# Optimization experiments

Measured on AMD Instinct MI355X. Metric: run time of the kernel, lower is better.

Reference implementation:

```python
import jax, jax.numpy as jnp
import numpy as np

D_MODEL = 1024
H = 16
D_K = D_MODEL // H


def setup_inputs() -> dict:
    key = jax.random.key(0)
    ks = jax.random.split(key, 12)
    B, S = 2, 2048
    inp = {
        "q": jax.random.normal(ks[0], (B, S, D_MODEL), jnp.float32),
        "k": jax.random.normal(ks[1], (B, S, D_MODEL), jnp.float32),
        "v": jax.random.normal(ks[2], (B, S, D_MODEL), jnp.float32),
        "mask": jax.random.randint(ks[3], (1, 1, S, S), 0, 2, jnp.int32),
    }
    s = 1.0 / np.sqrt(D_MODEL)
    inp["wq_w"] = jax.random.normal(ks[4], (D_MODEL, D_MODEL), jnp.float32) * s
    inp["wq_b"] = jnp.zeros((D_MODEL,), jnp.float32)
    inp["wk_w"] = jax.random.normal(ks[5], (D_MODEL, D_MODEL), jnp.float32) * s
    inp["wk_b"] = jnp.zeros((D_MODEL,), jnp.float32)
    inp["wv_w"] = jax.random.normal(ks[6], (D_MODEL, D_MODEL), jnp.float32) * s
    inp["wv_b"] = jnp.zeros((D_MODEL,), jnp.float32)
    inp["wo_w"] = jax.random.normal(ks[7], (D_MODEL, D_MODEL), jnp.float32) * s
    inp["wo_b"] = jnp.zeros((D_MODEL,), jnp.float32)
    return inp


def reference(q, k, v, mask, wq_w, wq_b, wk_w, wk_b, wv_w, wv_b, wo_w, wo_b):
    B, S, _ = q.shape
    # projections (torch Linear: x @ W^T + b)
    def proj(x, w, b):
        y = x @ w.T + b
        return y.reshape(B, S, H, D_K).transpose(0, 2, 1, 3)  # [B,H,S,Dk]

    Q = proj(q, wq_w, wq_b)
    K = proj(k, wk_w, wk_b)
    V = proj(v, wv_w, wv_b)

    scores = jnp.einsum("bhqd,bhkd->bhqk", Q, K) / jnp.sqrt(jnp.float32(D_K))
    # source quirk: masked positions set to 1e-9 (NOT -inf) before softmax
    scores = jnp.where(mask == 0, jnp.float32(1e-9), scores)
    attn = jax.nn.softmax(scores, axis=-1)
    out = jnp.einsum("bhqk,bhkd->bhqd", attn, V)
    out = out.transpose(0, 2, 1, 3).reshape(B, S, H * D_K)
    return out @ wo_w.T + wo_b
```

## Files before the change

kernel.cpp:

```cpp
#include <hip/hip_runtime.h>

typedef _Float16 half_t;
typedef _Float16 h8 __attribute__((ext_vector_type(8)));
typedef _Float16 h4 __attribute__((ext_vector_type(4)));
typedef _Float16 h2 __attribute__((ext_vector_type(2)));
typedef float f32x4 __attribute__((ext_vector_type(4)));
typedef float f32x16 __attribute__((ext_vector_type(16)));

#define S_LEN 2048
#define DMODEL 1024
#define NHEAD 16
#define HDK 64
#define NB 2
#define MROWS (NB * S_LEN)
#define LOG2E 1.44269504089f

__device__ __forceinline__ void gload_lds16(const void* g, void* l) {
  __builtin_amdgcn_global_load_lds(
      (const __attribute__((address_space(1))) unsigned int*)g,
      (__attribute__((address_space(3))) unsigned int*)l, 16, 0, 0);
}

__device__ __forceinline__ float fast_exp2(float x) {
  float r;
  asm("v_exp_f32 %0, %1" : "=v"(r) : "v"(x));
  return r;
}

__device__ __forceinline__ int swz(int row, int colByte) {
  return row * 128 + (colByte ^ ((row & 7) << 4));
}

__global__ __launch_bounds__(256) void pre_kernel(
    const float* __restrict__ q, const float* __restrict__ k, const float* __restrict__ v,
    const float* __restrict__ wq, const float* __restrict__ wk,
    const float* __restrict__ wv, const float* __restrict__ wo,
    const int* __restrict__ mask,
    half_t* Xq, half_t* Xk, half_t* Xv,
    half_t* Wq, half_t* Wk, half_t* Wv, half_t* Wo,
    unsigned int* mbits) {
  const int gid = blockIdx.x, tid = threadIdx.x;
  if (gid < 16384) {
    int i = gid * 256 + tid;
    const float* src; half_t* dst; int off;
    if (i < 3145728) {
      int rgn = i >> 20; off = i & 1048575;
      src = rgn == 0 ? q : rgn == 1 ? k : v;
      dst = rgn == 0 ? Xq : rgn == 1 ? Xk : Xv;
    } else {
      int j = i - 3145728;
      int rgn = j >> 18; off = j & 262143;
      src = rgn == 0 ? wq : rgn == 1 ? wk : rgn == 2 ? wv : wo;
      dst = rgn == 0 ? Wq : rgn == 1 ? Wk : rgn == 2 ? Wv : Wo;
    }
    float4 vv = ((const float4*)src)[off];
    h4 o;
    o[0] = (half_t)vv.x; o[1] = (half_t)vv.y; o[2] = (half_t)vv.z; o[3] = (half_t)vv.w;
    ((h4*)dst)[off] = o;
  } else {
    int i = (gid - 16384) * 256 + tid;
    int mv = mask[i];
    unsigned long long bm = __ballot(mv != 0);
    int lane = tid & 63;
    if (lane == 0)       mbits[i >> 5] = (unsigned int)bm;
    else if (lane == 32) mbits[i >> 5] = (unsigned int)(bm >> 32);
  }
}

template <int EPI>
__global__ __launch_bounds__(256) void gemm_kernel(
    const half_t* __restrict__ A0, const half_t* __restrict__ A1, const half_t* __restrict__ A2,
    const half_t* __restrict__ W0, const half_t* __restrict__ W1, const half_t* __restrict__ W2,
    const float* __restrict__ b0, const float* __restrict__ b1, const float* __restrict__ b2,
    void* o0, void* o1, void* o2) {
  const half_t* A; const half_t* W; const float* bias; void* out; float scale;
  if (blockIdx.z == 0)      { A = A0; W = W0; bias = b0; out = o0; scale = (EPI == 0) ? 0.125f * LOG2E : 1.0f; }
  else if (blockIdx.z == 1) { A = A1; W = W1; bias = b1; out = o1; scale = 1.0f; }
  else                      { A = A2; W = W2; bias = b2; out = o2; scale = 1.0f; }

  __shared__ half_t As[128 * 32];
  __shared__ half_t Bs[128 * 32];
  const int tid = threadIdx.x;
  const int w = tid >> 6, lane = tid & 63;
  const int wm = w >> 1, wn = w & 1;
  const int bm = blockIdx.x, bn = blockIdx.y;
  const int crow = lane >> 2;
  const int ck = (lane & 3) * 8;

  f32x4 acc[4][4] = {};

  const half_t* Ag0 = A + (size_t)(bm * 128 + w * 16 + crow) * DMODEL + ck;
  const half_t* Ag1 = Ag0 + 64 * DMODEL;
  const half_t* Wg0 = W + (size_t)(bn * 128 + w * 16 + crow) * DMODEL + ck;
  const half_t* Wg1 = Wg0 + 64 * DMODEL;
  half_t* lA0 = As + w * 512;
  half_t* lA1 = As + (w + 4) * 512;
  half_t* lB0 = Bs + w * 512;
  half_t* lB1 = Bs + (w + 4) * 512;

  for (int kt = 0; kt < DMODEL; kt += 32) {
    __syncthreads();
    gload_lds16(Ag0 + kt, lA0);
    gload_lds16(Ag1 + kt, lA1);
    gload_lds16(Wg0 + kt, lB0);
    gload_lds16(Wg1 + kt, lB1);
    __syncthreads();

    h8 af[4], bf[4];
    const int rr = lane & 15;
    const int kk = (lane >> 4) * 8;
#pragma unroll
    for (int i = 0; i < 4; ++i)
      af[i] = *(const h8*)(As + (wm * 64 + i * 16 + rr) * 32 + kk);
#pragma unroll
    for (int j = 0; j < 4; ++j)
      bf[j] = *(const h8*)(Bs + (wn * 64 + j * 16 + rr) * 32 + kk);
#pragma unroll
    for (int i = 0; i < 4; ++i)
#pragma unroll
      for (int j = 0; j < 4; ++j)
        acc[i][j] = __builtin_amdgcn_mfma_f32_16x16x32_f16(af[i], bf[j], acc[i][j], 0, 0, 0);
  }

  const int r0 = bm * 128 + wm * 64;
  const int c0 = bn * 128 + wn * 64;
#pragma unroll
  for (int j = 0; j < 4; ++j) {
    int col = c0 + j * 16 + (lane & 15);
    float bc = bias[col];
#pragma unroll
    for (int i = 0; i < 4; ++i) {
#pragma unroll
      for (int jj = 0; jj < 4; ++jj) {
        int row = r0 + i * 16 + (lane >> 4) * 4 + jj;
        float val = acc[i][j][jj] + bc;
        if (EPI == 0) {
          int bb = row >> 11, s = row & (S_LEN - 1);
          int hh = col >> 6, dk = col & 63;
          if (blockIdx.z == 2) {
            ((half_t*)out)[((size_t)((bb * NHEAD + hh) * HDK + dk)) * S_LEN + s] = (half_t)val;
          } else {
            ((half_t*)out)[(((size_t)(bb * NHEAD + hh)) * S_LEN + s) * HDK + dk] =
                (half_t)(val * scale);
          }
        } else {
          ((float*)out)[(size_t)row * DMODEL + col] = val;
        }
      }
    }
  }
}

__global__ __launch_bounds__(512, 2) void attn_kernel(
    const half_t* __restrict__ Qp, const half_t* __restrict__ Kp,
    const half_t* __restrict__ VTp, const unsigned int* __restrict__ mbits,
    half_t* __restrict__ AO) {
  __shared__ char smem[65536];

  const int tid = threadIdx.x, w = tid >> 6, lane = tid & 63;
  const int kvhalf = w >> 2, wq = w & 3;
  const int id = blockIdx.x;
  const int xcd = id & 7, rr = id >> 3;
  const int qt = rr & 15;
  const int bh = (xcd << 2) | (rr >> 4);
  const int b = bh >> 4, h = bh & 15;
  const int q32 = lane & 31, hi = lane >> 5;
  const int qbase = qt * 128 + wq * 32;
  const int kvbase = kvhalf * 16;
  const half_t* Qb = Qp + (size_t)bh * (S_LEN * HDK);
  const char* Kb = (const char*)(Kp + (size_t)bh * (S_LEN * HDK));
  const char* VTb = (const char*)(VTp + (size_t)bh * (S_LEN * HDK));
  const unsigned int* mrow = mbits + (size_t)(qbase + q32) * (S_LEN / 32);

  char* KsS = smem + kvhalf * 16384;
  char* VsS = smem + 32768 + kvhalf * 16384;

  const int srow = wq * 16 + (lane >> 3);
  const int scb = (lane & 7) * 16;

  h8 qf[4];
#pragma unroll
  for (int s = 0; s < 4; ++s)
    qf[s] = *(const h8*)(Qb + (size_t)(qbase + q32) * HDK + s * 16 + hi * 8);

  f32x16 acc0 = {}, acc1 = {};
  float l_run = 0.f;

  unsigned int mwA = mrow[kvbase * 2], mwB = mrow[kvbase * 2 + 1];
#pragma unroll
  for (int p = 0; p < 2; ++p) {
    int r = srow + p * 8;
    gload_lds16(Kb + (size_t)(kvbase * 64 + r) * 128 + (scb ^ ((r & 7) << 4)),
                KsS + (wq * 16 + p * 8) * 128);
    gload_lds16(VTb + (size_t)r * (S_LEN * 2) + kvbase * 128 + (scb ^ ((r & 7) << 4)),
                VsS + (wq * 16 + p * 8) * 128);
  }
  __syncthreads();

  int cur = 0;
  for (int t = 0; t < 16; ++t) {
    const unsigned int mw0 = mwA >> (hi * 4);
    const unsigned int mw1 = mwB >> (hi * 4);

    if (t < 15) {
      const int kvn = kvbase + t + 1;
#pragma unroll
      for (int p = 0; p < 2; ++p) {
        int r = srow + p * 8;
        gload_lds16(Kb + (size_t)(kvn * 64 + r) * 128 + (scb ^ ((r & 7) << 4)),
                    KsS + (cur ^ 1) * 8192 + (wq * 16 + p * 8) * 128);
        gload_lds16(VTb + (size_t)r * (S_LEN * 2) + kvn * 128 + (scb ^ ((r & 7) << 4)),
                    VsS + (cur ^ 1) * 8192 + (wq * 16 + p * 8) * 128);
      }
      mwA = mrow[kvn * 2];
      mwB = mrow[kvn * 2 + 1];
    }

    const char* kb = KsS + cur * 8192;
    const char* vb = VsS + cur * 8192;
    f32x16 sc0 = {}, sc1 = {};
    __builtin_amdgcn_s_setprio(1);
#pragma unroll
    for (int s = 0; s < 4; ++s) {
      h8 kf0 = *(const h8*)(kb + swz(q32, s * 32 + hi * 16));
      h8 kf1 = *(const h8*)(kb + swz(32 + q32, s * 32 + hi * 16));
      sc0 = __builtin_amdgcn_mfma_f32_32x32x16_f16(kf0, qf[s], sc0, 0, 0, 0);
      sc1 = __builtin_amdgcn_mfma_f32_32x32x16_f16(kf1, qf[s], sc1, 0, 0, 0);
    }
    __builtin_amdgcn_s_setprio(0);

#pragma unroll
    for (int rg = 0; rg < 16; ++rg) {
      const int bit = (rg & 3) + 8 * (rg >> 2);
      float p0 = fast_exp2(((mw0 >> bit) & 1u) ? sc0[rg] : 0.0f);
      float p1 = fast_exp2(((mw1 >> bit) & 1u) ? sc1[rg] : 0.0f);
      sc0[rg] = p0; sc1[rg] = p1;
      l_run += p0 + p1;
    }

#pragma unroll
    for (int s = 0; s < 4; ++s) {
      f32x16& P = (s < 2) ? sc0 : sc1;
      const int rb = (s & 1) * 8;
      union { h2 h; unsigned int u; } c01, c23, c45, c67;
      c01.h[0] = (half_t)P[rb + 0]; c01.h[1] = (half_t)P[rb + 1];
      c23.h[0] = (half_t)P[rb + 2]; c23.h[1] = (half_t)P[rb + 3];
      c45.h[0] = (half_t)P[rb + 4]; c45.h[1] = (half_t)P[rb + 5];
      c67.h[0] = (half_t)P[rb + 6]; c67.h[1] = (half_t)P[rb + 7];
      auto rA = __builtin_amdgcn_permlane32_swap(c01.u, c45.u, false, false);
      auto rB = __builtin_amdgcn_permlane32_swap(c23.u, c67.u, false, false);
      union { unsigned int u[4]; h8 v; } bw;
      bw.u[0] = rA[0]; bw.u[1] = rB[0]; bw.u[2] = rA[1]; bw.u[3] = rB[1];

      h8 vf0 = *(const h8*)(vb + swz(q32, s * 32 + hi * 16));
      h8 vf1 = *(const h8*)(vb + swz(32 + q32, s * 32 + hi * 16));
      __builtin_amdgcn_s_setprio(1);
      acc0 = __builtin_amdgcn_mfma_f32_32x32x16_f16(vf0, bw.v, acc0, 0, 0, 0);
      acc1 = __builtin_amdgcn_mfma_f32_32x32x16_f16(vf1, bw.v, acc1, 0, 0, 0);
      __builtin_amdgcn_s_setprio(0);
    }

    __syncthreads();
    cur ^= 1;
  }

  float* my = (float*)smem + (wq * 64 + lane) * 33;
  if (kvhalf) {
#pragma unroll
    for (int rg = 0; rg < 16; ++rg) { my[rg] = acc0[rg]; my[16 + rg] = acc1[rg]; }
    my[32] = l_run;
  }
  __syncthreads();
  if (!kvhalf) {
#pragma unroll
    for (int rg = 0; rg < 16; ++rg) { acc0[rg] += my[rg]; acc1[rg] += my[16 + rg]; }
    l_run += my[32];
    l_run += __shfl_xor(l_run, 32);

    const float inv = 1.0f / l_run;
    const int qrow = qbase + q32;
    half_t* aob = AO + (size_t)(b * S_LEN + qrow) * DMODEL + h * HDK;
#pragma unroll
    for (int rq = 0; rq < 4; ++rq) {
      h4 s0, s1;
#pragma unroll
      for (int j = 0; j < 4; ++j) {
        s0[j] = (half_t)(acc0[rq * 4 + j] * inv);
        s1[j] = (half_t)(acc1[rq * 4 + j] * inv);
      }
      const int d0 = 8 * rq + 4 * hi;
      *(h4*)(aob + d0) = s0;
      *(h4*)(aob + 32 + d0) = s1;
    }
  }
}

extern "C" void kernel_launch(void* const* d_in, const int* in_sizes, int n_in,
                              void* d_out, int out_size, void* d_ws, size_t ws_size,
                              hipStream_t stream) {
  const float* q    = (const float*)d_in[0];
  const float* k    = (const float*)d_in[1];
  const float* v    = (const float*)d_in[2];
  const int*   mask = (const int*)d_in[3];
  const float* wq_w = (const float*)d_in[4];
  const float* wq_b = (const float*)d_in[5];
  const float* wk_w = (const float*)d_in[6];
  const float* wk_b = (const float*)d_in[7];
  const float* wv_w = (const float*)d_in[8];
  const float* wv_b = (const float*)d_in[9];
  const float* wo_w = (const float*)d_in[10];
  const float* wo_b = (const float*)d_in[11];
  float* out = (float*)d_out;

  char* ws = (char*)d_ws;
  const size_t MB = (size_t)1 << 20;
  half_t* Xq = (half_t*)(ws + 0 * MB);
  half_t* Xk = (half_t*)(ws + 8 * MB);
  half_t* Xv = (half_t*)(ws + 16 * MB);
  half_t* Wq = (half_t*)(ws + 24 * MB);
  half_t* Wk = (half_t*)(ws + 26 * MB);
  half_t* Wv = (half_t*)(ws + 28 * MB);
  half_t* Wo = (half_t*)(ws + 30 * MB);
  half_t* Qp = (half_t*)(ws + 32 * MB);
  half_t* Kp = (half_t*)(ws + 40 * MB);
  half_t* VT = (half_t*)(ws + 48 * MB);
  unsigned int* mbits = (unsigned int*)(ws + 56 * MB);
  half_t* AO = Xq;

  pre_kernel<<<32768, 256, 0, stream>>>(q, k, v, wq_w, wk_w, wv_w, wo_w, mask,
                                        Xq, Xk, Xv, Wq, Wk, Wv, Wo, mbits);
  gemm_kernel<0><<<dim3(32, 8, 3), 256, 0, stream>>>(
      Xq, Xk, Xv, Wq, Wk, Wv, wq_b, wk_b, wv_b, (void*)Qp, (void*)Kp, (void*)VT);
  attn_kernel<<<512, 512, 0, stream>>>(Qp, Kp, VT, mbits, AO);
  gemm_kernel<1><<<dim3(32, 8, 1), 256, 0, stream>>>(
      AO, AO, AO, Wo, Wo, Wo, wo_b, wo_b, wo_b, (void*)out, (void*)out, (void*)out);

  (void)in_sizes; (void)n_in; (void)out_size; (void)ws_size;
}
```

Measured before the change: 146.6 us.

## Fuse fp32-to-fp16 activation conversion into QKV GEMM and restructure attention blocks

The QKV projection GEMM now reads the fp32 q/k/v activations directly, converts them to fp16 in registers and stores them to LDS. This removes the separate pre-pass that wrote fp16 copies of the activations, along with its extra global traffic. The attention kernel moves from 512-thread blocks with two KV halves to 256-thread blocks with 64-query tiles, 32 KV steps and 32KB LDS, giving twice as many blocks and higher occupancy. The trade-off is that the GEMM's A-tile load becomes a synchronous register path instead of an async global-to-LDS load, which may stall the GEMM.

Result: faster. 142.1 us (-3.1%).

```diff
diff --git a/kernel.cpp b/kernel.cpp
--- a/kernel.cpp
+++ b/kernel.cpp
@@ -32,33 +32,23 @@
 }
 
 __global__ __launch_bounds__(256) void pre_kernel(
-    const float* __restrict__ q, const float* __restrict__ k, const float* __restrict__ v,
     const float* __restrict__ wq, const float* __restrict__ wk,
     const float* __restrict__ wv, const float* __restrict__ wo,
     const int* __restrict__ mask,
-    half_t* Xq, half_t* Xk, half_t* Xv,
     half_t* Wq, half_t* Wk, half_t* Wv, half_t* Wo,
     unsigned int* mbits) {
   const int gid = blockIdx.x, tid = threadIdx.x;
-  if (gid < 16384) {
+  if (gid < 4096) {
     int i = gid * 256 + tid;
-    const float* src; half_t* dst; int off;
-    if (i < 3145728) {
-      int rgn = i >> 20; off = i & 1048575;
-      src = rgn == 0 ? q : rgn == 1 ? k : v;
-      dst = rgn == 0 ? Xq : rgn == 1 ? Xk : Xv;
-    } else {
-      int j = i - 3145728;
-      int rgn = j >> 18; off = j & 262143;
-      src = rgn == 0 ? wq : rgn == 1 ? wk : rgn == 2 ? wv : wo;
-      dst = rgn == 0 ? Wq : rgn == 1 ? Wk : rgn == 2 ? Wv : Wo;
-    }
+    int rgn = i >> 18, off = i & 262143;
+    const float* src = rgn == 0 ? wq : rgn == 1 ? wk : rgn == 2 ? wv : wo;
+    half_t* dst = rgn == 0 ? Wq : rgn == 1 ? Wk : rgn == 2 ? Wv : Wo;
     float4 vv = ((const float4*)src)[off];
     h4 o;
     o[0] = (half_t)vv.x; o[1] = (half_t)vv.y; o[2] = (half_t)vv.z; o[3] = (half_t)vv.w;
     ((h4*)dst)[off] = o;
   } else {
-    int i = (gid - 16384) * 256 + tid;
+    int i = (gid - 4096) * 256 + tid;
     int mv = mask[i];
     unsigned long long bm = __ballot(mv != 0);
     int lane = tid & 63;
@@ -69,11 +59,11 @@
 
 template <int EPI>
 __global__ __launch_bounds__(256) void gemm_kernel(
-    const half_t* __restrict__ A0, const half_t* __restrict__ A1, const half_t* __restrict__ A2,
+    const void* A0, const void* A1, const void* A2,
     const half_t* __restrict__ W0, const half_t* __restrict__ W1, const half_t* __restrict__ W2,
     const float* __restrict__ b0, const float* __restrict__ b1, const float* __restrict__ b2,
     void* o0, void* o1, void* o2) {
-  const half_t* A; const half_t* W; const float* bias; void* out; float scale;
+  const void* A; const half_t* W; const float* bias; void* out; float scale;
   if (blockIdx.z == 0)      { A = A0; W = W0; bias = b0; out = o0; scale = (EPI == 0) ? 0.125f * LOG2E : 1.0f; }
   else if (blockIdx.z == 1) { A = A1; W = W1; bias = b1; out = o1; scale = 1.0f; }
   else                      { A = A2; W = W2; bias = b2; out = o2; scale = 1.0f; }
@@ -89,8 +79,10 @@
 
   f32x4 acc[4][4] = {};
 
-  const half_t* Ag0 = A + (size_t)(bm * 128 + w * 16 + crow) * DMODEL + ck;
-  const half_t* Ag1 = Ag0 + 64 * DMODEL;
+  const float* Af0 = (const float*)A + (size_t)(bm * 128 + w * 16 + crow) * DMODEL + ck;
+  const float* Af1 = Af0 + 64 * DMODEL;
+  const half_t* Ah0 = (const half_t*)A + (size_t)(bm * 128 + w * 16 + crow) * DMODEL + ck;
+  const half_t* Ah1 = Ah0 + 64 * DMODEL;
   const half_t* Wg0 = W + (size_t)(bn * 128 + w * 16 + crow) * DMODEL + ck;
   const half_t* Wg1 = Wg0 + 64 * DMODEL;
   half_t* lA0 = As + w * 512;
@@ -100,10 +92,24 @@
 
   for (int kt = 0; kt < DMODEL; kt += 32) {
     __syncthreads();
-    gload_lds16(Ag0 + kt, lA0);
-    gload_lds16(Ag1 + kt, lA1);
     gload_lds16(Wg0 + kt, lB0);
     gload_lds16(Wg1 + kt, lB1);
+    if (EPI == 0) {
+      float4 x0 = *(const float4*)(Af0 + kt);
+      float4 x1 = *(const float4*)(Af0 + kt + 4);
+      float4 y0 = *(const float4*)(Af1 + kt);
+      float4 y1 = *(const float4*)(Af1 + kt + 4);
+      h8 ha, hb;
+      ha[0] = (half_t)x0.x; ha[1] = (half_t)x0.y; ha[2] = (half_t)x0.z; ha[3] = (half_t)x0.w;
+      ha[4] = (half_t)x1.x; ha[5] = (half_t)x1.y; ha[6] = (half_t)x1.z; ha[7] = (half_t)x1.w;
+      hb[0] = (half_t)y0.x; hb[1] = (half_t)y0.y; hb[2] = (half_t)y0.z; hb[3] = (half_t)y0.w;
+      hb[4] = (half_t)y1.x; hb[5] = (half_t)y1.y; hb[6] = (half_t)y1.z; hb[7] = (half_t)y1.w;
+      *(h8*)((char*)lA0 + (size_t)lane * 16) = ha;
+      *(h8*)((char*)lA1 + (size_t)lane * 16) = hb;
+    } else {
+      gload_lds16(Ah0 + kt, lA0);
+      gload_lds16(Ah1 + kt, lA1);
+    }
     __syncthreads();
 
     h8 af[4], bf[4];
@@ -151,31 +157,29 @@
   }
 }
 
-__global__ __launch_bounds__(512, 2) void attn_kernel(
+__global__ __launch_bounds__(256, 4) void attn_kernel(
     const half_t* __restrict__ Qp, const half_t* __restrict__ Kp,
     const half_t* __restrict__ VTp, const unsigned int* __restrict__ mbits,
     half_t* __restrict__ AO) {
-  __shared__ char smem[65536];
+  __shared__ char smem[32768];
 
   const int tid = threadIdx.x, w = tid >> 6, lane = tid & 63;
-  const int kvhalf = w >> 2, wq = w & 3;
+  const int qg = w >> 1, kh = w & 1;
   const int id = blockIdx.x;
-  const int xcd = id & 7, rr = id >> 3;
-  const int qt = rr & 15;
-  const int bh = (xcd << 2) | (rr >> 4);
+  const int xcd = id & 7, rest = id >> 3;
+  const int bh = (xcd << 2) | (rest >> 5);
+  const int qt = rest & 31;
   const int b = bh >> 4, h = bh & 15;
   const int q32 = lane & 31, hi = lane >> 5;
-  const int qbase = qt * 128 + wq * 32;
-  const int kvbase = kvhalf * 16;
+  const int qbase = qt * 64 + qg * 32;
   const half_t* Qb = Qp + (size_t)bh * (S_LEN * HDK);
   const char* Kb = (const char*)(Kp + (size_t)bh * (S_LEN * HDK));
   const char* VTb = (const char*)(VTp + (size_t)bh * (S_LEN * HDK));
   const unsigned int* mrow = mbits + (size_t)(qbase + q32) * (S_LEN / 32);
 
-  char* KsS = smem + kvhalf * 16384;
-  char* VsS = smem + 32768 + kvhalf * 16384;
-
-  const int srow = wq * 16 + (lane >> 3);
+  char* Ks = smem;
+  char* Vs = smem + 16384;
+  const int srow = w * 16 + (lane >> 3);
   const int scb = (lane & 7) * 16;
 
   h8 qf[4];
@@ -186,92 +190,93 @@
   f32x16 acc0 = {}, acc1 = {};
   float l_run = 0.f;
 
-  unsigned int mwA = mrow[kvbase * 2], mwB = mrow[kvbase * 2 + 1];
+  unsigned int mw = mrow[kh];
 #pragma unroll
   for (int p = 0; p < 2; ++p) {
     int r = srow + p * 8;
-    gload_lds16(Kb + (size_t)(kvbase * 64 + r) * 128 + (scb ^ ((r & 7) << 4)),
-                KsS + (wq * 16 + p * 8) * 128);
-    gload_lds16(VTb + (size_t)r * (S_LEN * 2) + kvbase * 128 + (scb ^ ((r & 7) << 4)),
-                VsS + (wq * 16 + p * 8) * 128);
+    gload_lds16(Kb + (size_t)r * 128 + (scb ^ ((r & 7) << 4)),
+                Ks + (w * 16 + p * 8) * 128);
+    gload_lds16(VTb + (size_t)r * (S_LEN * 2) + (scb ^ ((r & 7) << 4)),
+                Vs + (w * 16 + p * 8) * 128);
   }
   __syncthreads();
 
   int cur = 0;
-  for (int t = 0; t < 16; ++t) {
-    const unsigned int mw0 = mwA >> (hi * 4);
-    const unsigned int mw1 = mwB >> (hi * 4);
-
-    if (t < 15) {
-      const int kvn = kvbase + t + 1;
+  for (int t = 0; t < 32; ++t) {
+    const unsigned int mwc = mw >> (hi * 4);
+
+    if (t < 31) {
+      const int kvn = t + 1;
 #pragma unroll
       for (int p = 0; p < 2; ++p) {
         int r = srow + p * 8;
         gload_lds16(Kb + (size_t)(kvn * 64 + r) * 128 + (scb ^ ((r & 7) << 4)),
-                    KsS + (cur ^ 1) * 8192 + (wq * 16 + p * 8) * 128);
+                    Ks + (cur ^ 1) * 8192 + (w * 16 + p * 8) * 128);
         gload_lds16(VTb + (size_t)r * (S_LEN * 2) + kvn * 128 + (scb ^ ((r & 7) << 4)),
-                    VsS + (cur ^ 1) * 8192 + (wq * 16 + p * 8) * 128);
+                    Vs + (cur ^ 1) * 8192 + (w * 16 + p * 8) * 128);
       }
-      mwA = mrow[kvn * 2];
-      mwB = mrow[kvn * 2 + 1];
-    }
-
-    const char* kb = KsS + cur * 8192;
-    const char* vb = VsS + cur * 8192;
-    f32x16 sc0 = {}, sc1 = {};
+      mw = mrow[kvn * 2 + kh];
+    }
+
+    const char* kb = Ks + cur * 8192;
+    const char* vb = Vs + cur * 8192;
+    f32x16 sc = {};
     __builtin_amdgcn_s_setprio(1);
 #pragma unroll
     for (int s = 0; s < 4; ++s) {
-      h8 kf0 = *(const h8*)(kb + swz(q32, s * 32 + hi * 16));
-      h8 kf1 = *(const h8*)(kb + swz(32 + q32, s * 32 + hi * 16));
-      sc0 = __builtin_amdgcn_mfma_f32_32x32x16_f16(kf0, qf[s], sc0, 0, 0, 0);
-      sc1 = __builtin_amdgcn_mfma_f32_32x32x16_f16(kf1, qf[s], sc1, 0, 0, 0);
+      h8 kf = *(const h8*)(kb + swz(kh * 32 + q32, s * 32 + hi * 16));
+      sc = __builtin_amdgcn_mfma_f32_32x32x16_f16(kf, qf[s], sc, 0, 0, 0);
     }
     __builtin_amdgcn_s_setprio(0);
+
+    h8 vf00 = *(const h8*)(vb + swz(q32, kh * 64 + hi * 16));
+    h8 vf01 = *(const h8*)(vb + swz(q32, kh * 64 + 32 + hi * 16));
+    h8 vf10 = *(const h8*)(vb + swz(32 + q32, kh * 64 + hi * 16));
+    h8 vf11 = *(const h8*)(vb + swz(32 + q32, kh * 64 + 32 + hi * 16));
 
 #pragma unroll
     for (int rg = 0; rg < 16; ++rg) {
       const int bit = (rg & 3) + 8 * (rg >> 2);
-      float p0 = fast_exp2(((mw0 >> bit) & 1u) ? sc0[rg] : 0.0f);
-      float p1 = fast_exp2(((mw1 >> bit) & 1u) ? sc1[rg] : 0.0f);
-      sc0[rg] = p0; sc1[rg] = p1;
-      l_run += p0 + p1;
-    }
-
-#pragma unroll
-    for (int s = 0; s < 4; ++s) {
-      f32x16& P = (s < 2) ? sc0 : sc1;
-      const int rb = (s & 1) * 8;
+      float p = fast_exp2(((mwc >> bit) & 1u) ? sc[rg] : 0.0f);
+      sc[rg] = p;
+      l_run += p;
+    }
+
+    h8 pb[2];
+#pragma unroll
+    for (int s = 0; s < 2; ++s) {
+      const int rb = s * 8;
       union { h2 h; unsigned int u; } c01, c23, c45, c67;
-      c01.h[0] = (half_t)P[rb + 0]; c01.h[1] = (half_t)P[rb + 1];
-      c23.h[0] = (half_t)P[rb + 2]; c23.h[1] = (half_t)P[rb + 3];
-      c45.h[0] = (half_t)P[rb + 4]; c45.h[1] = (half_t)P[rb + 5];
-      c67.h[0] = (half_t)P[rb + 6]; c67.h[1] = (half_t)P[rb + 7];
+      c01.h[0] = (half_t)sc[rb + 0]; c01.h[1] = (half_t)sc[rb + 1];
+      c23.h[0] = (half_t)sc[rb + 2]; c23.h[1] = (half_t)sc[rb + 3];
+      c45.h[0] = (half_t)sc[rb + 4]; c45.h[1] = (half_t)sc[rb + 5];
+      c67.h[0] = (half_t)sc[rb + 6]; c67.h[1] = (half_t)sc[rb + 7];
       auto rA = __builtin_amdgcn_permlane32_swap(c01.u, c45.u, false, false);
       auto rB = __builtin_amdgcn_permlane32_swap(c23.u, c67.u, false, false);
       union { unsigned int u[4]; h8 v; } bw;
       bw.u[0] = rA[0]; bw.u[1] = rB[0]; bw.u[2] = rA[1]; bw.u[3] = rB[1];
-
-      h8 vf0 = *(const h8*)(vb + swz(q32, s * 32 + hi * 16));
-      h8 vf1 = *(const h8*)(vb + swz(32 + q32, s * 32 + hi * 16));
-      __builtin_amdgcn_s_setprio(1);
-      acc0 = __builtin_amdgcn_mfma_f32_32x32x16_f16(vf0, bw.v, acc0, 0, 0, 0);
-      acc1 = __builtin_amdgcn_mfma_f32_32x32x16_f16(vf1, bw.v, acc1, 0, 0, 0);
-      __builtin_amdgcn_s_setprio(0);
-    }
+      pb[s] = bw.v;
+    }
+
+    __builtin_amdgcn_s_setprio(1);
+    acc0 = __builtin_amdgcn_mfma_f32_32x32x16_f16(vf00, pb[0], acc0, 0, 0, 0);
+    acc1 = __builtin_amdgcn_mfma_f32_32x32x16_f16(vf10, pb[0], acc1, 0, 0, 0);
+    acc0 = __builtin_amdgcn_mfma_f32_32x32x16_f16(vf01, pb[1], acc0, 0, 0, 0);
+    acc1 = __builtin_amdgcn_mfma_f32_32x32x16_f16(vf11, pb[1], acc1, 0, 0, 0);
+    __builtin_amdgcn_s_setprio(0);
 
     __syncthreads();
     cur ^= 1;
   }
 
-  float* my = (float*)smem + (wq * 64 + lane) * 33;
-  if (kvhalf) {
+  float* my = (float*)smem + (qg * 64 + lane) * 33;
+  if (kh) {
 #pragma unroll
     for (int rg = 0; rg < 16; ++rg) { my[rg] = acc0[rg]; my[16 + rg] = acc1[rg]; }
     my[32] = l_run;
   }
   __syncthreads();
-  if (!kvhalf) {
+  if (!kh) {
 #pragma unroll
     for (int rg = 0; rg < 16; ++rg) { acc0[rg] += my[rg]; acc1[rg] += my[16 + rg]; }
     l_run += my[32];
@@ -314,9 +319,7 @@
 
   char* ws = (char*)d_ws;
   const size_t MB = (size_t)1 << 20;
-  half_t* Xq = (half_t*)(ws + 0 * MB);
-  half_t* Xk = (half_t*)(ws + 8 * MB);
-  half_t* Xv = (half_t*)(ws + 16 * MB);
+  half_t* AO = (half_t*)(ws + 0 * MB);
   half_t* Wq = (half_t*)(ws + 24 * MB);
   half_t* Wk = (half_t*)(ws + 26 * MB);
   half_t* Wv = (half_t*)(ws + 28 * MB);
@@ -325,13 +328,12 @@
   half_t* Kp = (half_t*)(ws + 40 * MB);
   half_t* VT = (half_t*)(ws + 48 * MB);
   unsigned int* mbits = (unsigned int*)(ws + 56 * MB);
-  half_t* AO = Xq;
-
-  pre_kernel<<<32768, 256, 0, stream>>>(q, k, v, wq_w, wk_w, wv_w, wo_w, mask,
-                                        Xq, Xk, Xv, Wq, Wk, Wv, Wo, mbits);
+
+  pre_kernel<<<20480, 256, 0, stream>>>(wq_w, wk_w, wv_w, wo_w, mask,
+                                        Wq, Wk, Wv, Wo, mbits);
   gemm_kernel<0><<<dim3(32, 8, 3), 256, 0, stream>>>(
-      Xq, Xk, Xv, Wq, Wk, Wv, wq_b, wk_b, wv_b, (void*)Qp, (void*)Kp, (void*)VT);
-  attn_kernel<<<512, 512, 0, stream>>>(Qp, Kp, VT, mbits, AO);
+      q, k, v, Wq, Wk, Wv, wq_b, wk_b, wv_b, (void*)Qp, (void*)Kp, (void*)VT);
+  attn_kernel<<<1024, 256, 0, stream>>>(Qp, Kp, VT, mbits, AO);
   gemm_kernel<1><<<dim3(32, 8, 1), 256, 0, stream>>>(
       AO, AO, AO, Wo, Wo, Wo, wo_b, wo_b, wo_b, (void*)out, (void*)out, (void*)out);
 
```
